# Performance work log

Measured on AMD Instinct MI355X. Metric: run time of the kernel, lower is better.

The kernel has to match this reference:

```python
import jax, jax.numpy as jnp
import numpy as np

S, B, D, HID, OUT = 96, 16, 512, 128, 2


def setup_inputs() -> dict:
    key = jax.random.key(0)
    ks = jax.random.split(key, 6)
    embeds = jax.random.normal(ks[0], (S, B, D), dtype=jnp.float32)
    embeds_cmp = jax.random.normal(ks[1], (S, B, D), dtype=jnp.float32)
    umask = jnp.ones((B, S), dtype=jnp.float32)   # unused by the math
    qmask = jnp.zeros((S, B, 2), dtype=jnp.float32)  # unused by the math
    # fc: Linear(2*D -> HID); classify: Linear(HID -> OUT)
    W1 = jax.random.normal(ks[2], (HID, 2 * D), dtype=jnp.float32) * 0.02
    b1 = jnp.zeros((HID,), dtype=jnp.float32)
    W2 = jax.random.normal(ks[3], (OUT, HID), dtype=jnp.float32) * 0.02
    b2 = jnp.zeros((OUT,), dtype=jnp.float32)
    return {"embeds": embeds, "umask": umask, "qmask": qmask,
            "embeds_cmp": embeds_cmp, "W1": W1, "b1": b1, "W2": W2, "b2": b2}


def reference(embeds, umask, qmask, embeds_cmp, W1, b1, W2, b2):
    # Pairwise concat [embeds_i ; embeds_cmp_j] -> Linear(2D->HID).
    # Split W1 into halves so the quadratic concat is never materialized:
    # concat(x1,x2) @ W1^T == x1 @ W1a^T + x2 @ W1b^T (same math, fused form).
    d = embeds.shape[-1]
    W1a, W1b = W1[:, :d], W1[:, d:]
    ha = jnp.einsum('ibd,hd->ibh', embeds, W1a)        # [S,B,HID]
    hb = jnp.einsum('jbd,hd->jbh', embeds_cmp, W1b)    # [S,B,HID]
    h = jax.nn.relu(ha[:, None] + hb[None, :] + b1)    # [S,S,B,HID]
    # Dropout(p=0.9) is identity in eval mode.
    logits = jnp.einsum('ijbh,ch->ijbc', h, W2) + b2   # [S,S,B,2]
    return logits
```

## Files before the change

kernel.cpp:

```cpp
#include <hip/hip_runtime.h>

#define S_   96
#define B_   16
#define D_   512
#define HID_ 128
#define M_   (S_ * B_)

typedef __attribute__((ext_vector_type(4))) float        f32x4_t;
typedef __attribute__((ext_vector_type(2))) float        f32x2_t;
typedef __attribute__((ext_vector_type(4))) unsigned int u32x4_t;
typedef __attribute__((ext_vector_type(8))) short        short8;

static __device__ __forceinline__ void split8(f32x4_t a, f32x4_t b,
                                              short8& hi, short8& lo) {
    float f[8];
    #pragma unroll
    for (int j = 0; j < 4; ++j) { f[j] = a[j]; f[4 + j] = b[j]; }
    unsigned int hb[8], lb[8];
    #pragma unroll
    for (int j = 0; j < 8; ++j) {
        unsigned int u = __float_as_uint(f[j]);
        float hf = __uint_as_float(u & 0xffff0000u);
        hb[j] = u >> 16;
        lb[j] = __float_as_uint(f[j] - hf) >> 16;
    }
    union { u32x4_t u; short8 s; } H, L;
    #pragma unroll
    for (int j = 0; j < 4; ++j) {
        H.u[j] = hb[2 * j] | (hb[2 * j + 1] << 16);
        L.u[j] = lb[2 * j] | (lb[2 * j + 1] << 16);
    }
    hi = H.s; lo = L.s;
}

__global__ __launch_bounds__(256) void stage1_mfma(
    const float* __restrict__ emb,
    const float* __restrict__ embc,
    const float* __restrict__ W1,
    const float* __restrict__ b1,
    float* __restrict__ ws)
{
    const int wave = threadIdx.x >> 6;
    const int lane = threadIdx.x & 63;
    const int gm = blockIdx.x * 64 + wave * 16;
    const int z  = (gm >= M_) ? 1 : 0;
    const int m0 = gm - z * M_;
    const int n0 = blockIdx.y * 16;

    const int rsel = lane & 15;
    const int kq   = (lane >> 4) * 8;
    const float* xr = (z ? embc : emb) + (m0 + rsel) * D_ + kq;
    const float* wr = W1 + (n0 + rsel) * (2 * D_) + z * D_ + kq;

    f32x4_t acc = {0.f, 0.f, 0.f, 0.f};
    #pragma unroll
    for (int k = 0; k < D_; k += 32) {
        f32x4_t xa = *(const f32x4_t*)(xr + k);
        f32x4_t xb = *(const f32x4_t*)(xr + k + 4);
        f32x4_t wa = *(const f32x4_t*)(wr + k);
        f32x4_t wb = *(const f32x4_t*)(wr + k + 4);
        short8 xhi, xlo, whi, wlo;
        split8(xa, xb, xhi, xlo);
        split8(wa, wb, whi, wlo);
        acc = __builtin_amdgcn_mfma_f32_16x16x32_bf16(xhi, whi, acc, 0, 0, 0);
        acc = __builtin_amdgcn_mfma_f32_16x16x32_bf16(xhi, wlo, acc, 0, 0, 0);
        acc = __builtin_amdgcn_mfma_f32_16x16x32_bf16(xlo, whi, acc, 0, 0, 0);
    }

    const int h = n0 + rsel;
    const float bias = z ? 0.f : b1[h];
    const int mrow = m0 + (lane >> 4) * 4;
    float* dst = ws + (size_t)z * (M_ * HID_);
    #pragma unroll
    for (int r = 0; r < 4; ++r) {
        dst[(mrow + r) * HID_ + h] = acc[r] + bias;
    }
}

__global__ __launch_bounds__(256) void stage2(
    const float* __restrict__ ws,
    const float* __restrict__ W2,
    const float* __restrict__ b2,
    float* __restrict__ out)
{
    __shared__ float ha_s[16 * 132];
    __shared__ float hb_s[16 * 132];
    __shared__ float w2_s[2 * HID_];

    const int t  = threadIdx.x;
    const int i0 = blockIdx.x * 16;
    const int j0 = blockIdx.y * 16;
    const int b  = blockIdx.z;

    {
        const int r = t >> 4;
        const int c = (t & 15) * 8;
        const float* pHa = ws + ((i0 + r) * B_ + b) * HID_ + c;
        const float* pHb = ws + (M_ * HID_) + ((j0 + r) * B_ + b) * HID_ + c;
        *(f32x4_t*)&ha_s[r * 132 + c]     = *(const f32x4_t*)pHa;
        *(f32x4_t*)&ha_s[r * 132 + c + 4] = *(const f32x4_t*)(pHa + 4);
        *(f32x4_t*)&hb_s[r * 132 + c]     = *(const f32x4_t*)pHb;
        *(f32x4_t*)&hb_s[r * 132 + c + 4] = *(const f32x4_t*)(pHb + 4);
        w2_s[t] = W2[t];
    }
    __syncthreads();

    const int ti = t >> 4, tj = t & 15;
    const float* pa = &ha_s[ti * 132];
    const float* pb = &hb_s[tj * 132];
    float acc0 = 0.f, acc1 = 0.f;
    #pragma unroll
    for (int h = 0; h < HID_; h += 4) {
        f32x4_t av = *(const f32x4_t*)(pa + h);
        f32x4_t bv = *(const f32x4_t*)(pb + h);
        f32x4_t w0 = *(const f32x4_t*)&w2_s[h];
        f32x4_t w1 = *(const f32x4_t*)&w2_s[HID_ + h];
        #pragma unroll
        for (int q = 0; q < 4; ++q) {
            float v = fmaxf(av[q] + bv[q], 0.f);
            acc0 = fmaf(v, w0[q], acc0);
            acc1 = fmaf(v, w1[q], acc1);
        }
    }

    const int i = i0 + ti, j = j0 + tj;
    const int idx = ((i * S_ + j) * B_ + b) * 2;
    f32x2_t o = { acc0 + b2[0], acc1 + b2[1] };
    *(f32x2_t*)(out + idx) = o;
}

__global__ __launch_bounds__(256) void fused_fallback(
    const float* __restrict__ emb,
    const float* __restrict__ embc,
    const float* __restrict__ W1,
    const float* __restrict__ b1,
    const float* __restrict__ W2,
    const float* __restrict__ b2,
    float* __restrict__ out)
{
    __shared__ float ha_s[16 * 132];
    __shared__ float hb_s[16 * 132];
    __shared__ float w2_s[2 * HID_];

    const int t  = threadIdx.x;
    const int i0 = blockIdx.x * 16;
    const int j0 = blockIdx.y * 16;
    const int b  = blockIdx.z;

    w2_s[t] = W2[t];

    for (int o = t; o < 4096; o += 256) {
        const int side = o >> 11;
        const int mi   = (o >> 7) & 15;
        const int h    = o & 127;
        const int srow = ((side ? j0 : i0) + mi) * B_ + b;
        const float* x = (side ? embc : emb) + srow * D_;
        const float* w = W1 + h * (2 * D_) + side * D_;
        float s = side ? 0.f : b1[h];
        for (int d = 0; d < D_; d += 4) {
            f32x4_t xv = *(const f32x4_t*)(x + d);
            f32x4_t wv = *(const f32x4_t*)(w + d);
            s = fmaf(xv[0], wv[0], s);
            s = fmaf(xv[1], wv[1], s);
            s = fmaf(xv[2], wv[2], s);
            s = fmaf(xv[3], wv[3], s);
        }
        (side ? hb_s : ha_s)[mi * 132 + h] = s;
    }
    __syncthreads();

    const int ti = t >> 4, tj = t & 15;
    const float* pa = &ha_s[ti * 132];
    const float* pb = &hb_s[tj * 132];
    float acc0 = 0.f, acc1 = 0.f;
    #pragma unroll
    for (int h = 0; h < HID_; h += 4) {
        f32x4_t av = *(const f32x4_t*)(pa + h);
        f32x4_t bv = *(const f32x4_t*)(pb + h);
        f32x4_t w0 = *(const f32x4_t*)&w2_s[h];
        f32x4_t w1 = *(const f32x4_t*)&w2_s[HID_ + h];
        #pragma unroll
        for (int q = 0; q < 4; ++q) {
            float v = fmaxf(av[q] + bv[q], 0.f);
            acc0 = fmaf(v, w0[q], acc0);
            acc1 = fmaf(v, w1[q], acc1);
        }
    }
    const int i = i0 + ti, j = j0 + tj;
    const int idx = ((i * S_ + j) * B_ + b) * 2;
    f32x2_t ov = { acc0 + b2[0], acc1 + b2[1] };
    *(f32x2_t*)(out + idx) = ov;
}

extern "C" void kernel_launch(void* const* d_in, const int* in_sizes, int n_in,
                              void* d_out, int out_size, void* d_ws, size_t ws_size,
                              hipStream_t stream) {
    const float* emb  = (const float*)d_in[0];
    const float* embc = (const float*)d_in[3];
    const float* W1   = (const float*)d_in[4];
    const float* b1   = (const float*)d_in[5];
    const float* W2   = (const float*)d_in[6];
    const float* b2   = (const float*)d_in[7];
    float* out = (float*)d_out;

    const size_t need = (size_t)2 * M_ * HID_ * sizeof(float);
    if (d_ws != nullptr && ws_size >= need) {
        float* ws = (float*)d_ws;
        stage1_mfma<<<dim3(48, 8), 256, 0, stream>>>(emb, embc, W1, b1, ws);
        stage2<<<dim3(6, 6, 16), 256, 0, stream>>>(ws, W2, b2, out);
    } else {
        fused_fallback<<<dim3(6, 6, 16), 256, 0, stream>>>(emb, embc, W1, b1, W2, b2, out);
    }
}
```

Measured before the change: 91.19 us.

## Split stage1 GEMM along K into four chunks, reduce partials in stage2

Stage1's projection GEMM is split over the reduction dimension into four chunks via a third grid dimension, and each chunk writes its partial sums to its own workspace slice. Stage2 sums the four partials while loading its tiles into shared memory. The aim is to give stage1 four times as many blocks (384 to 1536) so the GPU's compute units are better occupied. The cost is four times the workspace traffic and a larger workspace requirement. If the workspace is too small, the code falls back to the slow fused kernel.

```diff
diff --git a/kernel.cpp b/kernel.cpp
--- a/kernel.cpp
+++ b/kernel.cpp
@@ -5,6 +5,9 @@
 #define D_   512
 #define HID_ 128
 #define M_   (S_ * B_)
+#define KC_  4
+#define KCH_ (D_ / KC_)
+#define CHF_ (2 * M_ * HID_)
 
 typedef __attribute__((ext_vector_type(4))) float        f32x4_t;
 typedef __attribute__((ext_vector_type(2))) float        f32x2_t;
@@ -46,15 +49,16 @@
     const int z  = (gm >= M_) ? 1 : 0;
     const int m0 = gm - z * M_;
     const int n0 = blockIdx.y * 16;
+    const int kc = blockIdx.z;
 
     const int rsel = lane & 15;
     const int kq   = (lane >> 4) * 8;
-    const float* xr = (z ? embc : emb) + (m0 + rsel) * D_ + kq;
-    const float* wr = W1 + (n0 + rsel) * (2 * D_) + z * D_ + kq;
+    const float* xr = (z ? embc : emb) + (m0 + rsel) * D_ + kc * KCH_ + kq;
+    const float* wr = W1 + (n0 + rsel) * (2 * D_) + z * D_ + kc * KCH_ + kq;
 
     f32x4_t acc = {0.f, 0.f, 0.f, 0.f};
     #pragma unroll
-    for (int k = 0; k < D_; k += 32) {
+    for (int k = 0; k < KCH_; k += 32) {
         f32x4_t xa = *(const f32x4_t*)(xr + k);
         f32x4_t xb = *(const f32x4_t*)(xr + k + 4);
         f32x4_t wa = *(const f32x4_t*)(wr + k);
@@ -68,9 +72,9 @@
     }
 
     const int h = n0 + rsel;
-    const float bias = z ? 0.f : b1[h];
+    const float bias = (z == 0 && kc == 0) ? b1[h] : 0.f;
     const int mrow = m0 + (lane >> 4) * 4;
-    float* dst = ws + (size_t)z * (M_ * HID_);
+    float* dst = ws + (size_t)kc * CHF_ + (size_t)z * (M_ * HID_);
     #pragma unroll
     for (int r = 0; r < 4; ++r) {
         dst[(mrow + r) * HID_ + h] = acc[r] + bias;
@@ -97,10 +101,19 @@
         const int c = (t & 15) * 8;
         const float* pHa = ws + ((i0 + r) * B_ + b) * HID_ + c;
         const float* pHb = ws + (M_ * HID_) + ((j0 + r) * B_ + b) * HID_ + c;
-        *(f32x4_t*)&ha_s[r * 132 + c]     = *(const f32x4_t*)pHa;
-        *(f32x4_t*)&ha_s[r * 132 + c + 4] = *(const f32x4_t*)(pHa + 4);
-        *(f32x4_t*)&hb_s[r * 132 + c]     = *(const f32x4_t*)pHb;
-        *(f32x4_t*)&hb_s[r * 132 + c + 4] = *(const f32x4_t*)(pHb + 4);
+        f32x4_t a0 = *(const f32x4_t*)pHa,       a1 = *(const f32x4_t*)(pHa + 4);
+        f32x4_t b0 = *(const f32x4_t*)pHb,       b1v = *(const f32x4_t*)(pHb + 4);
+        #pragma unroll
+        for (int kc = 1; kc < KC_; ++kc) {
+            const float* qa = pHa + (size_t)kc * CHF_;
+            const float* qb = pHb + (size_t)kc * CHF_;
+            a0  += *(const f32x4_t*)qa;       a1  += *(const f32x4_t*)(qa + 4);
+            b0  += *(const f32x4_t*)qb;       b1v += *(const f32x4_t*)(qb + 4);
+        }
+        *(f32x4_t*)&ha_s[r * 132 + c]     = a0;
+        *(f32x4_t*)&ha_s[r * 132 + c + 4] = a1;
+        *(f32x4_t*)&hb_s[r * 132 + c]     = b0;
+        *(f32x4_t*)&hb_s[r * 132 + c + 4] = b1v;
         w2_s[t] = W2[t];
     }
     __syncthreads();
@@ -203,10 +216,10 @@
     const float* b2   = (const float*)d_in[7];
     float* out = (float*)d_out;
 
-    const size_t need = (size_t)2 * M_ * HID_ * sizeof(float);
+    const size_t need = (size_t)KC_ * CHF_ * sizeof(float);
     if (d_ws != nullptr && ws_size >= need) {
         float* ws = (float*)d_ws;
-        stage1_mfma<<<dim3(48, 8), 256, 0, stream>>>(emb, embc, W1, b1, ws);
+        stage1_mfma<<<dim3(48, 8, KC_), 256, 0, stream>>>(emb, embc, W1, b1, ws);
         stage2<<<dim3(6, 6, 16), 256, 0, stream>>>(ws, W2, b2, out);
     } else {
         fused_fallback<<<dim3(6, 6, 16), 256, 0, stream>>>(emb, embc, W1, b1, W2, b2, out);
```

New measurement: 94.76 us. 3.9% more time.

## Stage GEMM tiles in LDS with pre-split bf16 and read W2 directly

Applied to the files above, without the earlier changes.

Stage1 now has each block load a 32x128 chunk of X and W1 into shared memory, splitting fp32 into bf16 hi/lo once per element. Four waves then share those tiles for 32x32 output per block instead of each wave loading and splitting its own 16x16 operands. This cuts redundant global loads and split work, at the cost of LDS traffic, two barriers per chunk and a different grid shape. Separately, stage2 and the fallback drop the W2 shared-memory copy and read W2 straight from global memory through the cache.

```diff
diff --git a/kernel.cpp b/kernel.cpp
--- a/kernel.cpp
+++ b/kernel.cpp
@@ -5,6 +5,8 @@
 #define D_   512
 #define HID_ 128
 #define M_   (S_ * B_)
+#define KCH_ 128
+#define LSTR_ 136
 
 typedef __attribute__((ext_vector_type(4))) float        f32x4_t;
 typedef __attribute__((ext_vector_type(2))) float        f32x2_t;
@@ -40,36 +42,67 @@
     const float* __restrict__ b1,
     float* __restrict__ ws)
 {
-    const int wave = threadIdx.x >> 6;
-    const int lane = threadIdx.x & 63;
-    const int gm = blockIdx.x * 64 + wave * 16;
-    const int z  = (gm >= M_) ? 1 : 0;
-    const int m0 = gm - z * M_;
-    const int n0 = blockIdx.y * 16;
+    __shared__ short x_hi[32 * LSTR_];
+    __shared__ short x_lo[32 * LSTR_];
+    __shared__ short w_hi[32 * LSTR_];
+    __shared__ short w_lo[32 * LSTR_];
+
+    const int t    = threadIdx.x;
+    const int wave = t >> 6;
+    const int lane = t & 63;
+    const int bx   = blockIdx.x;
+    const int h0   = blockIdx.y * 32;
+
+    const int z    = (bx >= 48) ? 1 : 0;
+    const int mloc = bx * 32 - z * M_;
+
+    const float* xbase = (z ? embc : emb) + (size_t)mloc * D_;
+    const float* wbase = W1 + (size_t)h0 * (2 * D_) + z * D_;
 
     const int rsel = lane & 15;
-    const int kq   = (lane >> 4) * 8;
-    const float* xr = (z ? embc : emb) + (m0 + rsel) * D_ + kq;
-    const float* wr = W1 + (n0 + rsel) * (2 * D_) + z * D_ + kq;
+    const int gq   = lane >> 4;
+    const int wm   = (wave & 1) * 16;
+    const int wh   = (wave >> 1) * 16;
 
     f32x4_t acc = {0.f, 0.f, 0.f, 0.f};
-    #pragma unroll
-    for (int k = 0; k < D_; k += 32) {
-        f32x4_t xa = *(const f32x4_t*)(xr + k);
-        f32x4_t xb = *(const f32x4_t*)(xr + k + 4);
-        f32x4_t wa = *(const f32x4_t*)(wr + k);
-        f32x4_t wb = *(const f32x4_t*)(wr + k + 4);
-        short8 xhi, xlo, whi, wlo;
-        split8(xa, xb, xhi, xlo);
-        split8(wa, wb, whi, wlo);
-        acc = __builtin_amdgcn_mfma_f32_16x16x32_bf16(xhi, whi, acc, 0, 0, 0);
-        acc = __builtin_amdgcn_mfma_f32_16x16x32_bf16(xhi, wlo, acc, 0, 0, 0);
-        acc = __builtin_amdgcn_mfma_f32_16x16x32_bf16(xlo, whi, acc, 0, 0, 0);
-    }
-
-    const int h = n0 + rsel;
+
+    for (int kc = 0; kc < D_; kc += KCH_) {
+        #pragma unroll
+        for (int rep = 0; rep < 2; ++rep) {
+            const int idx = rep * 256 + t;
+            const int row = idx >> 4;
+            const int g   = idx & 15;
+            short8 hi, lo;
+            const float* px = xbase + row * D_ + kc + g * 8;
+            split8(*(const f32x4_t*)px, *(const f32x4_t*)(px + 4), hi, lo);
+            *(short8*)&x_hi[row * LSTR_ + g * 8] = hi;
+            *(short8*)&x_lo[row * LSTR_ + g * 8] = lo;
+            const float* pw = wbase + row * (2 * D_) + kc + g * 8;
+            split8(*(const f32x4_t*)pw, *(const f32x4_t*)(pw + 4), hi, lo);
+            *(short8*)&w_hi[row * LSTR_ + g * 8] = hi;
+            *(short8*)&w_lo[row * LSTR_ + g * 8] = lo;
+        }
+        __syncthreads();
+
+        #pragma unroll
+        for (int kk = 0; kk < KCH_; kk += 32) {
+            const int goff = (kk >> 3) + gq;
+            const int oa = (wm + rsel) * LSTR_ + goff * 8;
+            const int ob = (wh + rsel) * LSTR_ + goff * 8;
+            short8 ahi = *(const short8*)&x_hi[oa];
+            short8 alo = *(const short8*)&x_lo[oa];
+            short8 bhi = *(const short8*)&w_hi[ob];
+            short8 blo = *(const short8*)&w_lo[ob];
+            acc = __builtin_amdgcn_mfma_f32_16x16x32_bf16(ahi, bhi, acc, 0, 0, 0);
+            acc = __builtin_amdgcn_mfma_f32_16x16x32_bf16(ahi, blo, acc, 0, 0, 0);
+            acc = __builtin_amdgcn_mfma_f32_16x16x32_bf16(alo, bhi, acc, 0, 0, 0);
+        }
+        __syncthreads();
+    }
+
+    const int h = h0 + wh + rsel;
     const float bias = z ? 0.f : b1[h];
-    const int mrow = m0 + (lane >> 4) * 4;
+    const int mrow = mloc + wm + (lane >> 4) * 4;
     float* dst = ws + (size_t)z * (M_ * HID_);
     #pragma unroll
     for (int r = 0; r < 4; ++r) {
@@ -85,7 +118,6 @@
 {
     __shared__ float ha_s[16 * 132];
     __shared__ float hb_s[16 * 132];
-    __shared__ float w2_s[2 * HID_];
 
     const int t  = threadIdx.x;
     const int i0 = blockIdx.x * 16;
@@ -101,7 +133,6 @@
         *(f32x4_t*)&ha_s[r * 132 + c + 4] = *(const f32x4_t*)(pHa + 4);
         *(f32x4_t*)&hb_s[r * 132 + c]     = *(const f32x4_t*)pHb;
         *(f32x4_t*)&hb_s[r * 132 + c + 4] = *(const f32x4_t*)(pHb + 4);
-        w2_s[t] = W2[t];
     }
     __syncthreads();
 
@@ -113,8 +144,8 @@
     for (int h = 0; h < HID_; h += 4) {
         f32x4_t av = *(const f32x4_t*)(pa + h);
         f32x4_t bv = *(const f32x4_t*)(pb + h);
-        f32x4_t w0 = *(const f32x4_t*)&w2_s[h];
-        f32x4_t w1 = *(const f32x4_t*)&w2_s[HID_ + h];
+        f32x4_t w0 = *(const f32x4_t*)(W2 + h);
+        f32x4_t w1 = *(const f32x4_t*)(W2 + HID_ + h);
         #pragma unroll
         for (int q = 0; q < 4; ++q) {
             float v = fmaxf(av[q] + bv[q], 0.f);
@@ -140,14 +171,11 @@
 {
     __shared__ float ha_s[16 * 132];
     __shared__ float hb_s[16 * 132];
-    __shared__ float w2_s[2 * HID_];
 
     const int t  = threadIdx.x;
     const int i0 = blockIdx.x * 16;
     const int j0 = blockIdx.y * 16;
     const int b  = blockIdx.z;
-
-    w2_s[t] = W2[t];
 
     for (int o = t; o < 4096; o += 256) {
         const int side = o >> 11;
@@ -177,8 +205,8 @@
     for (int h = 0; h < HID_; h += 4) {
         f32x4_t av = *(const f32x4_t*)(pa + h);
         f32x4_t bv = *(const f32x4_t*)(pb + h);
-        f32x4_t w0 = *(const f32x4_t*)&w2_s[h];
-        f32x4_t w1 = *(const f32x4_t*)&w2_s[HID_ + h];
+        f32x4_t w0 = *(const f32x4_t*)(W2 + h);
+        f32x4_t w1 = *(const f32x4_t*)(W2 + HID_ + h);
         #pragma unroll
         for (int q = 0; q < 4; ++q) {
             float v = fmaxf(av[q] + bv[q], 0.f);
@@ -206,7 +234,7 @@
     const size_t need = (size_t)2 * M_ * HID_ * sizeof(float);
     if (d_ws != nullptr && ws_size >= need) {
         float* ws = (float*)d_ws;
-        stage1_mfma<<<dim3(48, 8), 256, 0, stream>>>(emb, embc, W1, b1, ws);
+        stage1_mfma<<<dim3(96, 4), 256, 0, stream>>>(emb, embc, W1, b1, ws);
         stage2<<<dim3(6, 6, 16), 256, 0, stream>>>(ws, W2, b2, out);
     } else {
         fused_fallback<<<dim3(6, 6, 16), 256, 0, stream>>>(emb, embc, W1, b1, W2, b2, out);
```

Result: faster. 83.41 us (-8.5%).
